# Performance work log

Measured on AMD Instinct MI355X. Metric: run time of the kernel, lower is better.

Reference implementation:

```python
import jax, jax.numpy as jnp
import numpy as np

B, T, C, H = 8, 2048, 1024, 128


def setup_inputs() -> dict:
    key = jax.random.key(0)
    k1, k2, k3, k4 = jax.random.split(key, 4)
    x = jax.random.normal(k1, (B, T, C), dtype=jnp.float32)
    # Linear(n_embd, head_size, bias=False): weight is [head_size, n_embd] in torch,
    # applied as x @ W.T; we store W already transposed as [C, H].
    s = 1.0 / np.sqrt(C)
    Wk = jax.random.normal(k2, (C, H), dtype=jnp.float32) * s
    Wq = jax.random.normal(k3, (C, H), dtype=jnp.float32) * s
    Wv = jax.random.normal(k4, (C, H), dtype=jnp.float32) * s
    return {"x": x, "Wk": Wk, "Wq": Wq, "Wv": Wv}


def reference(x, Wk, Wq, Wv):
    # k, q, v projections
    k = jnp.einsum("btc,ch->bth", x, Wk)
    q = jnp.einsum("btc,ch->bth", x, Wq)
    v = jnp.einsum("btc,ch->bth", x, Wv)
    scale = k.shape[-1] ** -0.5
    wei = jnp.einsum("bqh,bkh->bqk", q, k) * scale  # [B,T,T]
    # causal mask: tril == 0 -> -inf
    Tq = x.shape[1]
    causal = jnp.tril(jnp.ones((Tq, Tq), dtype=bool))
    wei = jnp.where(causal, wei, -jnp.inf)
    wei = jax.nn.softmax(wei, axis=-1)
    # dropout p=0.0 -> identity
    out = jnp.einsum("bqk,bkh->bqh", wei, v)  # [B,T,H]
    return out
```

## Files before the change

kernel.cpp:

```cpp
#include <hip/hip_runtime.h>

typedef unsigned short u16;
typedef __attribute__((ext_vector_type(8))) short bf16x8;
typedef __attribute__((ext_vector_type(4))) float f32x4;
typedef __attribute__((ext_vector_type(4))) unsigned int u32x4;
typedef __attribute__((ext_vector_type(2))) unsigned int u32x2;

#define MFMA16(a, b, c) __builtin_amdgcn_mfma_f32_16x16x32_bf16((a), (b), (c), 0, 0, 0)

static constexpr int Bn = 8, Tn = 2048, Cn = 1024, Hn = 128;

static __device__ __forceinline__ u16 f2bf(float f) {
  union { float f; unsigned u; } v;
  v.f = f;
  unsigned r = v.u + 0x7fffu + ((v.u >> 16) & 1u);
  return (u16)(r >> 16);
}

static __device__ __forceinline__ float bf2f(u16 h) {
  union { unsigned u; float f; } v;
  v.u = ((unsigned)h) << 16;
  return v.f;
}

static __device__ __forceinline__ unsigned pack2(float a, float b) {
  return (unsigned)f2bf(a) | ((unsigned)f2bf(b) << 16);
}

__global__ __launch_bounds__(256) void wt_kernel(const float* __restrict__ Wk,
                                                 const float* __restrict__ Wq,
                                                 const float* __restrict__ Wv,
                                                 u16* __restrict__ Wt) {
  __shared__ u16 tile[64][65];
  const int c0 = blockIdx.x * 64;
  const int h0 = blockIdx.y * 64;
  const int z = blockIdx.z;
  const float* W = (z == 0) ? Wk : (z == 1) ? Wq : Wv;
  u16* dst = Wt + (size_t)z * Hn * Cn;
  const int tx = threadIdx.x & 63;
  const int ty = threadIdx.x >> 6;
#pragma unroll
  for (int i = 0; i < 16; ++i) {
    int r = ty * 16 + i;
    tile[r][tx] = f2bf(W[(size_t)(c0 + r) * Hn + h0 + tx]);
  }
  __syncthreads();
#pragma unroll
  for (int i = 0; i < 16; ++i) {
    int r = ty * 16 + i;
    dst[(size_t)(h0 + r) * Cn + c0 + tx] = tile[tx][r];
  }
}

__global__ __launch_bounds__(512, 4) void proj_kernel(const float* __restrict__ X,
                                                      const u16* __restrict__ Wt,
                                                      u16* __restrict__ Kb,
                                                      u16* __restrict__ Qb,
                                                      u16* __restrict__ Vt) {
  __shared__ u16 Xs[64][72];
  __shared__ u16 Ws[384][72];

  const int m0 = blockIdx.x * 64;
  const int tid = threadIdx.x;
  const int w = tid >> 6;
  const int wm = w & 1;
  const int wh = w >> 1;
  const int lane = tid & 63;
  const int l15 = lane & 15, lg = lane >> 4;

  const int xr = tid >> 3;
  const int xc = (tid & 7) * 8;
  const float* xptr = X + (size_t)(m0 + xr) * Cn + xc;
  const u16* wptr = Wt + (size_t)xr * Cn + xc;

  f32x4 acc[6][2] = {};
  f32x4 xl0, xl1;
  bf16x8 wl[6];

  xl0 = *reinterpret_cast<const f32x4*>(xptr);
  xl1 = *reinterpret_cast<const f32x4*>(xptr + 4);
#pragma unroll
  for (int i = 0; i < 6; ++i)
    wl[i] = *reinterpret_cast<const bf16x8*>(wptr + (size_t)i * 64 * Cn);

  for (int kt = 0; kt < Cn; kt += 64) {
    __syncthreads();
    {
      union { u16 h[8]; bf16x8 v; } cv;
#pragma unroll
      for (int j = 0; j < 4; ++j) {
        cv.h[j] = f2bf(xl0[j]);
        cv.h[4 + j] = f2bf(xl1[j]);
      }
      *reinterpret_cast<bf16x8*>(&Xs[xr][xc]) = cv.v;
#pragma unroll
      for (int i = 0; i < 6; ++i)
        *reinterpret_cast<bf16x8*>(&Ws[xr + i * 64][xc]) = wl[i];
    }
    if (kt + 64 < Cn) {
      xl0 = *reinterpret_cast<const f32x4*>(xptr + kt + 64);
      xl1 = *reinterpret_cast<const f32x4*>(xptr + kt + 64 + 4);
#pragma unroll
      for (int i = 0; i < 6; ++i)
        wl[i] = *reinterpret_cast<const bf16x8*>(wptr + (size_t)i * 64 * Cn + kt + 64);
    }
    __syncthreads();
#pragma unroll
    for (int kk = 0; kk < 2; ++kk) {
      const int ko = kk * 32 + lg * 8;
      bf16x8 af[6], bfx[2];
#pragma unroll
      for (int hf = 0; hf < 6; ++hf)
        af[hf] = *reinterpret_cast<const bf16x8*>(&Ws[wh * 96 + hf * 16 + l15][ko]);
#pragma unroll
      for (int mf = 0; mf < 2; ++mf)
        bfx[mf] = *reinterpret_cast<const bf16x8*>(&Xs[wm * 32 + mf * 16 + l15][ko]);
#pragma unroll
      for (int hf = 0; hf < 6; ++hf)
#pragma unroll
        for (int mf = 0; mf < 2; ++mf)
          acc[hf][mf] = MFMA16(af[hf], bfx[mf], acc[hf][mf]);
    }
  }

#pragma unroll
  for (int hf = 0; hf < 6; ++hf) {
    const int habs = wh * 96 + hf * 16 + lg * 4;
    const int p = habs >> 7;
    const int h = habs & 127;
    const float sc = (p == 1) ? 0.08838834764831845f : 1.0f;
#pragma unroll
    for (int mf = 0; mf < 2; ++mf) {
      const int m = m0 + wm * 32 + mf * 16 + l15;
      union { u16 h4[4]; u32x2 v; } pk;
#pragma unroll
      for (int r = 0; r < 4; ++r) pk.h4[r] = f2bf(acc[hf][mf][r] * sc);
      if (p == 0) {
        *reinterpret_cast<u32x2*>(&Kb[(size_t)m * Hn + h]) = pk.v;
      } else if (p == 1) {
        *reinterpret_cast<u32x2*>(&Qb[(size_t)m * Hn + h]) = pk.v;
      } else {
        const int b = m >> 11, t = m & (Tn - 1);
#pragma unroll
        for (int r = 0; r < 4; ++r)
          Vt[((size_t)b * Hn + h + r) * Tn + t] = pk.h4[r];
      }
    }
  }
}

__global__ __launch_bounds__(512) void attn_kernel(const u16* __restrict__ Qb,
                                                   const u16* __restrict__ Kb,
                                                   const u16* __restrict__ Vt,
                                                   float* __restrict__ Out) {
  __shared__ u16 SM[77824];
  __shared__ float Ml[8][16];
  constexpr int VOFF = 34816;
  constexpr int PLOFF = 68608;

  const int batch = blockIdx.x & 7;
  const int sr = blockIdx.x >> 3;
  const int q0 = (63 - sr) << 5;
  const int tid = threadIdx.x;
  const int w = tid >> 6;
  const int sw = w >> 2;
  const int par = w & 3;
  const int lane = tid & 63;
  const int l15 = lane & 15, lg = lane >> 4;

  const size_t bt = (size_t)batch * Tn;
  const int qrow = q0 + sw * 16;
  const int q = qrow + l15;

  bf16x8 qb[4];
#pragma unroll
  for (int kk = 0; kk < 4; ++kk)
    qb[kk] = *reinterpret_cast<const bf16x8*>(&Qb[(bt + q) * Hn + kk * 32 + lg * 8]);

  f32x4 o[8] = {};
  float l_r = 0.f;

  const int nt = (q0 + 32 + 255) >> 8;

  u32x4 kreg[8], vreg[8];
#define ATTN_LOAD(KN)                                                          \
  _Pragma("unroll")                                                            \
  for (int i = 0; i < 8; ++i) {                                                \
    const int idx = tid + i * 512;                                             \
    const int kr = idx >> 4, kc = (idx & 15) * 8;                              \
    kreg[i] = *reinterpret_cast<const u32x4*>(&Kb[(bt + (KN) + kr) * Hn + kc]); \
    const int vr = idx >> 5, vc = (idx & 31) * 8;                              \
    vreg[i] = *reinterpret_cast<const u32x4*>(                                 \
        &Vt[((size_t)batch * Hn + vr) * Tn + (KN) + vc]);                      \
  }

#define ATTN_STAGE()                                                           \
  _Pragma("unroll")                                                            \
  for (int i = 0; i < 8; ++i) {                                                \
    const int idx = tid + i * 512;                                             \
    const int kr = idx >> 4, kc = (idx & 15) * 8;                              \
    *reinterpret_cast<u32x4*>(&SM[kr * 136 + kc]) = kreg[i];                   \
    const int vr = idx >> 5, vc = (idx & 31) * 8;                              \
    *reinterpret_cast<u32x4*>(&SM[VOFF + vr * 264 + vc]) = vreg[i];            \
  }

  ATTN_LOAD(0)

  for (int t = 0; t < nt; ++t) {
    __syncthreads();
    ATTN_STAGE()
    if (t + 1 < nt) ATTN_LOAD((t + 1) << 8)
    __syncthreads();
    const int k0 = t << 8;
    const int kbase = k0 + par * 64;
    if (kbase <= qrow) {
      f32x4 s[4] = {};
#pragma unroll
      for (int nf = 0; nf < 4; ++nf) {
#pragma unroll
        for (int kk = 0; kk < 4; ++kk) {
          bf16x8 ka = *reinterpret_cast<const bf16x8*>(
              &SM[(par * 64 + nf * 16 + l15) * 136 + kk * 32 + lg * 8]);
          s[nf] = MFMA16(ka, qb[kk], s[nf]);
        }
      }

      if (kbase + 63 > qrow) {
#pragma unroll
        for (int nf = 0; nf < 4; ++nf)
#pragma unroll
          for (int r = 0; r < 4; ++r)
            if (kbase + nf * 16 + lg * 4 + r > q) s[nf][r] = -1e30f;
      }

#pragma unroll
      for (int nf = 0; nf < 4; ++nf)
#pragma unroll
        for (int r = 0; r < 4; ++r) {
          s[nf][r] = __expf(s[nf][r] - 16.0f);
          l_r += s[nf][r];
        }

      u16* PlW = &SM[PLOFF + w * 1152];
#pragma unroll
      for (int nf = 0; nf < 4; ++nf) {
        u32x2 pv;
        pv.x = pack2(s[nf][0], s[nf][1]);
        pv.y = pack2(s[nf][2], s[nf][3]);
        *reinterpret_cast<u32x2*>(&PlW[l15 * 72 + nf * 16 + lg * 4]) = pv;
      }
      asm volatile("s_waitcnt lgkmcnt(0)" ::: "memory");
      __builtin_amdgcn_sched_barrier(0);
      bf16x8 pb[2];
#pragma unroll
      for (int ks = 0; ks < 2; ++ks)
        pb[ks] = *reinterpret_cast<const bf16x8*>(&PlW[l15 * 72 + ks * 32 + lg * 8]);

#pragma unroll
      for (int n = 0; n < 8; ++n) {
#pragma unroll
        for (int ks = 0; ks < 2; ++ks) {
          bf16x8 va = *reinterpret_cast<const bf16x8*>(
              &SM[VOFF + (n * 16 + l15) * 264 + par * 64 + ks * 32 + lg * 8]);
          o[n] = MFMA16(va, pb[ks], o[n]);
        }
      }
    }
  }

  l_r += __shfl_xor(l_r, 16);
  l_r += __shfl_xor(l_r, 32);

  __syncthreads();

#pragma unroll
  for (int n = 0; n < 8; ++n) {
    u32x2 ov;
    ov.x = pack2(o[n][0], o[n][1]);
    ov.y = pack2(o[n][2], o[n][3]);
    *reinterpret_cast<u32x2*>(&SM[w * 2176 + l15 * 136 + n * 16 + lg * 4]) = ov;
  }
  if (lg == 0) Ml[w][l15] = l_r;
  __syncthreads();

  {
    const int row = tid >> 4;
    const int h0 = (tid & 15) * 8;
    const int sw2 = row >> 4;
    const int r16 = row & 15;
    const int wb = sw2 * 4;
    float L = 0.f;
#pragma unroll
    for (int i = 0; i < 4; ++i) L += Ml[wb + i][r16];
    const float inv = 1.0f / L;
    float outv[8] = {};
#pragma unroll
    for (int i = 0; i < 4; ++i) {
      u32x4 ov = *reinterpret_cast<const u32x4*>(&SM[(wb + i) * 2176 + r16 * 136 + h0]);
#pragma unroll
      for (int j = 0; j < 4; ++j) {
        outv[2 * j] += bf2f((u16)(ov[j] & 0xffffu));
        outv[2 * j + 1] += bf2f((u16)(ov[j] >> 16));
      }
    }
#pragma unroll
    for (int j = 0; j < 8; ++j) outv[j] *= inv;
    float* op = &Out[(bt + q0 + row) * Hn + h0];
    *reinterpret_cast<f32x4*>(op) = *reinterpret_cast<const f32x4*>(&outv[0]);
    *reinterpret_cast<f32x4*>(op + 4) = *reinterpret_cast<const f32x4*>(&outv[4]);
  }
}

extern "C" void kernel_launch(void* const* d_in, const int* in_sizes, int n_in,
                              void* d_out, int out_size, void* d_ws, size_t ws_size,
                              hipStream_t stream) {
  const float* X = (const float*)d_in[0];
  const float* Wk = (const float*)d_in[1];
  const float* Wq = (const float*)d_in[2];
  const float* Wv = (const float*)d_in[3];

  char* ws = (char*)d_ws;
  u16* Wt = (u16*)(ws);
  u16* Kb = (u16*)(ws + 786432);
  u16* Qb = (u16*)(ws + 786432 + 4194304);
  u16* Vt = (u16*)(ws + 786432 + 2 * 4194304);
  float* Out = (float*)d_out;

  wt_kernel<<<dim3(16, 2, 3), 256, 0, stream>>>(Wk, Wq, Wv, Wt);
  proj_kernel<<<dim3(256), 512, 0, stream>>>(X, Wt, Kb, Qb, Vt);
  attn_kernel<<<dim3(512), 512, 0, stream>>>(Qb, Kb, Vt, Out);
}
```

Baseline: 68.08 us.

## Double-buffer attention K/V tiles via direct global-to-LDS loads with XOR swizzle

Replaces register-staged K/V loading (global to registers, then to LDS) with direct global_load_lds into two LDS buffers, using an XOR column swizzle instead of padding to avoid bank conflicts. The key tile shrinks from 256 to 128 so the two buffers fit in LDS, and each wave now handles 32 keys per step instead of 64. The aim is to cut register pressure and the staging writes, and to overlap the next tile's load with compute. In exchange there are twice as many loop iterations and barriers, and less MFMA work between each sync.

```diff
diff --git a/kernel.cpp b/kernel.cpp
--- a/kernel.cpp
+++ b/kernel.cpp
@@ -25,6 +25,12 @@
 
 static __device__ __forceinline__ unsigned pack2(float a, float b) {
   return (unsigned)f2bf(a) | ((unsigned)f2bf(b) << 16);
+}
+
+static __device__ __forceinline__ void gll16(const u16* g, u16* l) {
+  __builtin_amdgcn_global_load_lds(
+      (const __attribute__((address_space(1))) void*)g,
+      (__attribute__((address_space(3))) void*)l, 16, 0, 0);
 }
 
 __global__ __launch_bounds__(256) void wt_kernel(const float* __restrict__ Wk,
@@ -153,10 +159,10 @@
                                                    const u16* __restrict__ Kb,
                                                    const u16* __restrict__ Vt,
                                                    float* __restrict__ Out) {
-  __shared__ u16 SM[77824];
+  __shared__ u16 SM[70656];
   __shared__ float Ml[8][16];
-  constexpr int VOFF = 34816;
-  constexpr int PLOFF = 68608;
+  constexpr int VSOFF = 32768;
+  constexpr int PLOFF = 65536;
 
   const int batch = blockIdx.x & 7;
   const int sr = blockIdx.x >> 3;
@@ -180,98 +186,89 @@
   f32x4 o[8] = {};
   float l_r = 0.f;
 
-  const int nt = (q0 + 32 + 255) >> 8;
-
-  u32x4 kreg[8], vreg[8];
-#define ATTN_LOAD(KN)                                                          \
-  _Pragma("unroll")                                                            \
-  for (int i = 0; i < 8; ++i) {                                                \
-    const int idx = tid + i * 512;                                             \
-    const int kr = idx >> 4, kc = (idx & 15) * 8;                              \
-    kreg[i] = *reinterpret_cast<const u32x4*>(&Kb[(bt + (KN) + kr) * Hn + kc]); \
-    const int vr = idx >> 5, vc = (idx & 31) * 8;                              \
-    vreg[i] = *reinterpret_cast<const u32x4*>(                                 \
-        &Vt[((size_t)batch * Hn + vr) * Tn + (KN) + vc]);                      \
-  }
-
-#define ATTN_STAGE()                                                           \
-  _Pragma("unroll")                                                            \
-  for (int i = 0; i < 8; ++i) {                                                \
-    const int idx = tid + i * 512;                                             \
-    const int kr = idx >> 4, kc = (idx & 15) * 8;                              \
-    *reinterpret_cast<u32x4*>(&SM[kr * 136 + kc]) = kreg[i];                   \
-    const int vr = idx >> 5, vc = (idx & 31) * 8;                              \
-    *reinterpret_cast<u32x4*>(&SM[VOFF + vr * 264 + vc]) = vreg[i];            \
-  }
-
-  ATTN_LOAD(0)
+  const int nt = (q0 + 32 + 127) >> 7;
+
+#define AGLL(KN, BUF)                                                          \
+  {                                                                            \
+    _Pragma("unroll")                                                          \
+    for (int j = 0; j < 4; ++j) {                                              \
+      const int rl = w * 16 + j * 4 + (lane >> 4);                             \
+      const int cs = (lane & 15) ^ (rl & 15);                                  \
+      gll16(&Kb[(bt + (KN) + rl) * Hn + cs * 8],                               \
+            &SM[(BUF) * 16384 + (w * 16 + j * 4) * 128]);                      \
+      gll16(&Vt[((size_t)batch * Hn + rl) * Tn + (KN) + cs * 8],               \
+            &SM[VSOFF + (BUF) * 16384 + (w * 16 + j * 4) * 128]);              \
+    }                                                                          \
+  }
+
+  AGLL(0, 0)
+  asm volatile("s_waitcnt vmcnt(0)" ::: "memory");
+  __syncthreads();
 
   for (int t = 0; t < nt; ++t) {
-    __syncthreads();
-    ATTN_STAGE()
-    if (t + 1 < nt) ATTN_LOAD((t + 1) << 8)
-    __syncthreads();
-    const int k0 = t << 8;
-    const int kbase = k0 + par * 64;
+    const int cur = t & 1;
+    if (t + 1 < nt) AGLL((t + 1) << 7, cur ^ 1)
+
+    const int k0 = t << 7;
+    const int kbase = k0 + par * 32;
     if (kbase <= qrow) {
-      f32x4 s[4] = {};
-#pragma unroll
-      for (int nf = 0; nf < 4; ++nf) {
+      const int ksB = cur * 16384;
+      const int vsB = VSOFF + cur * 16384;
+      f32x4 s[2] = {};
+#pragma unroll
+      for (int nf = 0; nf < 2; ++nf) {
+        const int krow = par * 32 + nf * 16 + l15;
 #pragma unroll
         for (int kk = 0; kk < 4; ++kk) {
           bf16x8 ka = *reinterpret_cast<const bf16x8*>(
-              &SM[(par * 64 + nf * 16 + l15) * 136 + kk * 32 + lg * 8]);
+              &SM[ksB + krow * 128 + (((kk * 4 + lg) ^ l15) << 3)]);
           s[nf] = MFMA16(ka, qb[kk], s[nf]);
         }
       }
 
-      if (kbase + 63 > qrow) {
-#pragma unroll
-        for (int nf = 0; nf < 4; ++nf)
+      if (kbase + 31 > qrow) {
+#pragma unroll
+        for (int nf = 0; nf < 2; ++nf)
 #pragma unroll
           for (int r = 0; r < 4; ++r)
             if (kbase + nf * 16 + lg * 4 + r > q) s[nf][r] = -1e30f;
       }
 
 #pragma unroll
-      for (int nf = 0; nf < 4; ++nf)
+      for (int nf = 0; nf < 2; ++nf)
 #pragma unroll
         for (int r = 0; r < 4; ++r) {
           s[nf][r] = __expf(s[nf][r] - 16.0f);
           l_r += s[nf][r];
         }
 
-      u16* PlW = &SM[PLOFF + w * 1152];
-#pragma unroll
-      for (int nf = 0; nf < 4; ++nf) {
+      u16* PlW = &SM[PLOFF + w * 640];
+#pragma unroll
+      for (int nf = 0; nf < 2; ++nf) {
         u32x2 pv;
         pv.x = pack2(s[nf][0], s[nf][1]);
         pv.y = pack2(s[nf][2], s[nf][3]);
-        *reinterpret_cast<u32x2*>(&PlW[l15 * 72 + nf * 16 + lg * 4]) = pv;
+        *reinterpret_cast<u32x2*>(&PlW[l15 * 40 + nf * 16 + lg * 4]) = pv;
       }
       asm volatile("s_waitcnt lgkmcnt(0)" ::: "memory");
       __builtin_amdgcn_sched_barrier(0);
-      bf16x8 pb[2];
-#pragma unroll
-      for (int ks = 0; ks < 2; ++ks)
-        pb[ks] = *reinterpret_cast<const bf16x8*>(&PlW[l15 * 72 + ks * 32 + lg * 8]);
+      bf16x8 pb = *reinterpret_cast<const bf16x8*>(&PlW[l15 * 40 + lg * 8]);
 
 #pragma unroll
       for (int n = 0; n < 8; ++n) {
-#pragma unroll
-        for (int ks = 0; ks < 2; ++ks) {
-          bf16x8 va = *reinterpret_cast<const bf16x8*>(
-              &SM[VOFF + (n * 16 + l15) * 264 + par * 64 + ks * 32 + lg * 8]);
-          o[n] = MFMA16(va, pb[ks], o[n]);
-        }
-      }
-    }
+        const int vrow = n * 16 + l15;
+        bf16x8 va = *reinterpret_cast<const bf16x8*>(
+            &SM[vsB + vrow * 128 + (((par * 4 + lg) ^ l15) << 3)]);
+        o[n] = MFMA16(va, pb, o[n]);
+      }
+    }
+
+    asm volatile("s_waitcnt vmcnt(0)" ::: "memory");
+    __syncthreads();
   }
 
   l_r += __shfl_xor(l_r, 16);
   l_r += __shfl_xor(l_r, 32);
-
-  __syncthreads();
 
 #pragma unroll
   for (int n = 0; n < 8; ++n) {
```

Result: no change. 68.51 us (+0.6%).

## Stream projection weights into double-buffered LDS via global_load_lds with XOR swizzle

Applied to the files above, without the earlier changes.

The projection kernel now loads the bf16 weight tiles straight from global memory into LDS with the async global_load_lds builtin, double-buffered so the next K-slice arrives while the current one feeds the MFMAs. This drops the six register-staged weight vectors and their LDS stores, and uses an XOR swizzle in place of padding to avoid bank conflicts. The larger LDS footprint (about 105KB) may lower occupancy, and there is no explicit wait on the async loads before the barrier, so correctness depends on the compiler inserting vmcnt waits.

```diff
diff --git a/kernel.cpp b/kernel.cpp
--- a/kernel.cpp
+++ b/kernel.cpp
@@ -25,6 +25,12 @@
 
 static __device__ __forceinline__ unsigned pack2(float a, float b) {
   return (unsigned)f2bf(a) | ((unsigned)f2bf(b) << 16);
+}
+
+static __device__ __forceinline__ void gll16(const u16* g, u16* l) {
+  __builtin_amdgcn_global_load_lds(
+      (const __attribute__((address_space(1))) void*)g,
+      (__attribute__((address_space(3))) void*)l, 16, 0, 0);
 }
 
 __global__ __launch_bounds__(256) void wt_kernel(const float* __restrict__ Wk,
@@ -57,8 +63,8 @@
                                                       u16* __restrict__ Kb,
                                                       u16* __restrict__ Qb,
                                                       u16* __restrict__ Vt) {
-  __shared__ u16 Xs[64][72];
-  __shared__ u16 Ws[384][72];
+  __shared__ u16 SMp[53760];
+  constexpr int WSOFF = 4608;
 
   const int m0 = blockIdx.x * 64;
   const int tid = threadIdx.x;
@@ -71,50 +77,59 @@
   const int xr = tid >> 3;
   const int xc = (tid & 7) * 8;
   const float* xptr = X + (size_t)(m0 + xr) * Cn + xc;
-  const u16* wptr = Wt + (size_t)xr * Cn + xc;
 
   f32x4 acc[6][2] = {};
   f32x4 xl0, xl1;
-  bf16x8 wl[6];
+
+#define AWGLL(KT, BUF)                                                        \
+  _Pragma("unroll")                                                           \
+  for (int i = 0; i < 6; ++i) {                                               \
+    const int idx = tid + i * 512;                                            \
+    const int row = idx >> 3;                                                 \
+    const int cs = (idx & 7) ^ (row & 7);                                     \
+    gll16(&Wt[(size_t)row * Cn + (KT) + cs * 8],                              \
+          &SMp[WSOFF + (BUF) * 24576 + (w * 64 + i * 512) * 8]);              \
+  }
+
+#define STAGE_X()                                                             \
+  {                                                                           \
+    union { u16 h[8]; bf16x8 v; } cv;                                         \
+    _Pragma("unroll")                                                         \
+    for (int j = 0; j < 4; ++j) {                                             \
+      cv.h[j] = f2bf(xl0[j]);                                                 \
+      cv.h[4 + j] = f2bf(xl1[j]);                                             \
+    }                                                                         \
+    *reinterpret_cast<bf16x8*>(&SMp[xr * 72 + xc]) = cv.v;                    \
+  }
 
   xl0 = *reinterpret_cast<const f32x4*>(xptr);
   xl1 = *reinterpret_cast<const f32x4*>(xptr + 4);
-#pragma unroll
-  for (int i = 0; i < 6; ++i)
-    wl[i] = *reinterpret_cast<const bf16x8*>(wptr + (size_t)i * 64 * Cn);
+  AWGLL(0, 0)
 
   for (int kt = 0; kt < Cn; kt += 64) {
+    const int buf = (kt >> 6) & 1;
     __syncthreads();
-    {
-      union { u16 h[8]; bf16x8 v; } cv;
-#pragma unroll
-      for (int j = 0; j < 4; ++j) {
-        cv.h[j] = f2bf(xl0[j]);
-        cv.h[4 + j] = f2bf(xl1[j]);
-      }
-      *reinterpret_cast<bf16x8*>(&Xs[xr][xc]) = cv.v;
-#pragma unroll
-      for (int i = 0; i < 6; ++i)
-        *reinterpret_cast<bf16x8*>(&Ws[xr + i * 64][xc]) = wl[i];
-    }
+    STAGE_X()
+    __syncthreads();
     if (kt + 64 < Cn) {
       xl0 = *reinterpret_cast<const f32x4*>(xptr + kt + 64);
       xl1 = *reinterpret_cast<const f32x4*>(xptr + kt + 64 + 4);
-#pragma unroll
-      for (int i = 0; i < 6; ++i)
-        wl[i] = *reinterpret_cast<const bf16x8*>(wptr + (size_t)i * 64 * Cn + kt + 64);
-    }
-    __syncthreads();
+      AWGLL(kt + 64, buf ^ 1)
+    }
 #pragma unroll
     for (int kk = 0; kk < 2; ++kk) {
-      const int ko = kk * 32 + lg * 8;
       bf16x8 af[6], bfx[2];
 #pragma unroll
-      for (int hf = 0; hf < 6; ++hf)
-        af[hf] = *reinterpret_cast<const bf16x8*>(&Ws[wh * 96 + hf * 16 + l15][ko]);
+      for (int hf = 0; hf < 6; ++hf) {
+        const int wrow = wh * 96 + hf * 16 + l15;
+        af[hf] = *reinterpret_cast<const bf16x8*>(
+            &SMp[WSOFF + buf * 24576 + wrow * 64 +
+                 (((kk * 4 + lg) ^ (l15 & 7)) << 3)]);
+      }
 #pragma unroll
       for (int mf = 0; mf < 2; ++mf)
-        bfx[mf] = *reinterpret_cast<const bf16x8*>(&Xs[wm * 32 + mf * 16 + l15][ko]);
+        bfx[mf] = *reinterpret_cast<const bf16x8*>(
+            &SMp[(wm * 32 + mf * 16 + l15) * 72 + kk * 32 + lg * 8]);
 #pragma unroll
       for (int hf = 0; hf < 6; ++hf)
 #pragma unroll
```

Measured after the change: 67.15 us. About the same (-1.4%).
